# Kernel optimization log

Measured on AMD Instinct MI355X. Metric: run time of the kernel, lower is better.

## Reference

```python
import jax, jax.numpy as jnp
import numpy as np

N = 100000
E = 1600000
F_IN = 500
HID = 8
HEADS = 8
C = 7
NEG_SLOPE = 0.2


def setup_inputs() -> dict:
    key = jax.random.key(0)
    ks = jax.random.split(key, 10)
    x = jax.random.normal(ks[0], (N, F_IN), dtype=jnp.float32)
    edge_index = jax.random.randint(ks[1], (2, E), 0, N, dtype=jnp.int64)
    # conv1 params: lin [heads*hid, F_in], att_src/att_dst [heads, hid], bias [heads*hid]
    s1 = 1.0 / np.sqrt(F_IN)
    W1 = jax.random.normal(ks[2], (HEADS * HID, F_IN), dtype=jnp.float32) * s1
    att_src1 = jax.random.normal(ks[3], (HEADS, HID), dtype=jnp.float32) * 0.1
    att_dst1 = jax.random.normal(ks[4], (HEADS, HID), dtype=jnp.float32) * 0.1
    b1 = jnp.zeros((HEADS * HID,), dtype=jnp.float32)
    # conv2 params: in = heads*hid, out = heads*C (concat=True)
    s2 = 1.0 / np.sqrt(HEADS * HID)
    W2 = jax.random.normal(ks[5], (HEADS * C, HEADS * HID), dtype=jnp.float32) * s2
    att_src2 = jax.random.normal(ks[6], (HEADS, C), dtype=jnp.float32) * 0.1
    att_dst2 = jax.random.normal(ks[7], (HEADS, C), dtype=jnp.float32) * 0.1
    b2 = jnp.zeros((HEADS * C,), dtype=jnp.float32)
    return {"x": x, "edge_index": edge_index, "W1": W1, "att_src1": att_src1,
            "att_dst1": att_dst1, "b1": b1, "W2": W2, "att_src2": att_src2,
            "att_dst2": att_dst2, "b2": b2}


def _gat_layer(h_in, src, dst, W, a_src, a_dst, b, heads, out_ch):
    n = h_in.shape[0]
    h = (h_in @ W.T).reshape(n, heads, out_ch)                 # [N,H,D]
    alpha_s = jnp.sum(h * a_src[None], axis=-1)                # [N,H]
    alpha_d = jnp.sum(h * a_dst[None], axis=-1)                # [N,H]
    e = jax.nn.leaky_relu(alpha_s[src] + alpha_d[dst], NEG_SLOPE)  # [E,H]
    # segment softmax over incoming edges of each dst node
    emax = jax.ops.segment_max(e, dst, num_segments=n)
    ee = jnp.exp(e - emax[dst])
    denom = jax.ops.segment_sum(ee, dst, num_segments=n)
    alpha = ee / denom[dst]                                    # [E,H]
    msg = h[src] * alpha[:, :, None]                           # [E,H,D]
    out = jax.ops.segment_sum(msg, dst, num_segments=n)        # [N,H,D]
    return out.reshape(n, heads * out_ch) + b


def reference(x, edge_index, W1, att_src1, att_dst1, b1, W2, att_src2, att_dst2, b2):
    n = x.shape[0]
    # PyG GATConv adds self-loops by default
    loop = jnp.arange(n, dtype=edge_index.dtype)
    src = jnp.concatenate([edge_index[0], loop])
    dst = jnp.concatenate([edge_index[1], loop])
    # dropout(p=0.6) is identity in eval mode
    h = _gat_layer(x, src, dst, W1, att_src1, att_dst1, b1, HEADS, HID)
    h = jax.nn.elu(h)
    out = _gat_layer(h, src, dst, W2, att_src2, att_dst2, b2, HEADS, C)
    return out  # [N, heads*num_classes]
```

## Files before the change

### kernel.cpp

```cpp
#include <hip/hip_runtime.h>

#define NEG_SLOPE 0.2f

typedef __bf16 bf16x8 __attribute__((ext_vector_type(8)));
typedef float f32x4 __attribute__((ext_vector_type(4)));

__device__ __forceinline__ float eluf(float x) { return x > 0.f ? x : __expf(x) - 1.f; }
__device__ __forceinline__ float lreluf(float x) { return x > 0.f ? x : NEG_SLOPE * x; }
__device__ __forceinline__ float bflo(unsigned u) { return __uint_as_float(u << 16); }
__device__ __forceinline__ float bfhi(unsigned u) { return __uint_as_float(u & 0xffff0000u); }
__device__ __forceinline__ float bfval(unsigned short u) { return __uint_as_float((unsigned)u << 16); }

__device__ __forceinline__ void split8(const float4& p, const float4& q, bf16x8& hi, bf16x8& lo) {
  float v[8] = {p.x, p.y, p.z, p.w, q.x, q.y, q.z, q.w};
#pragma unroll
  for (int e = 0; e < 8; ++e) {
    __bf16 h = (__bf16)v[e];
    hi[e] = h;
    lo[e] = (__bf16)(v[e] - (float)h);
  }
}

__global__ __launch_bounds__(256) void k_zero(int4* __restrict__ p, int n4) {
  int i = blockIdx.x * 256 + threadIdx.x;
  if (i < n4) p[i] = (int4){0, 0, 0, 0};
}


__global__ __launch_bounds__(256) void k_fill_prep(const int* __restrict__ raw, int* __restrict__ cnt,
                                                   int* __restrict__ csr, int E, int CH,
                                                   const float* __restrict__ W1,
                                                   __bf16* __restrict__ b1h, __bf16* __restrict__ b1l,
                                                   const float* __restrict__ W2,
                                                   const float* __restrict__ as2, const float* __restrict__ ad2,
                                                   __bf16* __restrict__ b2h, __bf16* __restrict__ b2l) {
  if (blockIdx.x < 128) {
    int idx = blockIdx.x * 256 + threadIdx.x;
    if (idx < 32768) {
      int e = idx & 7;
      int lane = (idx >> 3) & 63;
      int nf = (idx >> 9) & 3;
      int ks = idx >> 11;
      int k = ks * 32 + (lane >> 4) * 8 + e;
      int col = nf * 16 + (lane & 15);
      float w = (k < 500) ? W1[(size_t)col * 500 + k] : 0.f;
      __bf16 hh = (__bf16)w;
      b1h[idx] = hh;
      b1l[idx] = (__bf16)(w - (float)hh);
    }
    if (idx < 5120) {
      int e = idx & 7;
      int lane = (idx >> 3) & 63;
      int nf = (idx >> 9) % 5;
      int ks = idx / 2560;
      int k = ks * 32 + (lane >> 4) * 8 + e;
      int c16 = lane & 15;
      float w = 0.f;
      if (nf < 4) {
        int col = nf * 16 + c16;
        if (col < 56) w = W2[(size_t)col * 64 + k];
      } else {
        const float* a = (c16 < 8) ? as2 : ad2;
        int h = c16 & 7;
        float s = 0.f;
#pragma unroll
        for (int d = 0; d < 7; ++d) s = fmaf(a[h * 7 + d], W2[(size_t)(h * 7 + d) * 64 + k], s);
        w = s;
      }
      __bf16 hh = (__bf16)w;
      b2h[idx] = hh;
      b2l[idx] = (__bf16)(w - (float)hh);
    }
    return;
  }
  int probe = 0;
#pragma unroll
  for (int t = 1; t < 64; t += 2) probe |= raw[t];
  const bool is32 = probe != 0;
  const int fid = blockIdx.x - 128;
  const int shard = fid & 7;
  const int chunk = fid >> 3;
  const int i0 = chunk * CH;
  const int i1 = min(i0 + CH, E);
  for (int idx = i0 + (int)threadIdx.x; idx < i1; idx += 256) {
    int d = is32 ? raw[E + idx] : raw[2 * (E + idx)];
    if (((d >> 13) & 7) != shard) continue;
    int s = is32 ? raw[idx] : raw[2 * idx];
    int pos = atomicAdd(&cnt[d], 1);
    if (pos < 64) csr[(size_t)d * 64 + pos] = s;
  }
}

__global__ __launch_bounds__(256) void k_gemm1_lds(const float* __restrict__ X, const bf16x8* __restrict__ Bhi,
                                                   const bf16x8* __restrict__ Blo,
                                                   const float* __restrict__ at_s, const float* __restrict__ at_d,
                                                   __bf16* __restrict__ outb,
                                                   __bf16* __restrict__ as1b, float* __restrict__ ad_, int M) {
  __shared__ __align__(16) float xs[2][2048];
  __shared__ __align__(16) __bf16 bs[2][4096];
  const int lane = threadIdx.x & 63;
  const int wid = threadIdx.x >> 6;
  const int row0 = blockIdx.x * 64;
  const int kgrp = lane >> 4;
  const int rloc = lane & 15;
  const int myrow = wid * 16 + rloc;

  const int ub = myrow * 128 + kgrp * 32;
  const int sw1 = (ub ^ ((myrow & 7) << 4)) >> 2;
  const int sw2 = ((ub + 16) ^ ((myrow & 7) << 4)) >> 2;

  int st_r[2], st_kf[2];
#pragma unroll
  for (int j = 0; j < 2; ++j) {
    int s = (wid * 2 + j) * 1024 + lane * 16;
    int r = s >> 7;
    int kb = (s & 127) ^ ((r & 7) << 4);
    st_r[j] = min(row0 + r, M - 1);
    st_kf[j] = kb >> 2;
  }

  auto stage = [&](int buf, int ks) {
#pragma unroll
    for (int j = 0; j < 2; ++j) {
      const float* src = X + (size_t)st_r[j] * 500 + ks * 32 + st_kf[j];
      __builtin_amdgcn_global_load_lds(
          (const __attribute__((address_space(1))) void*)src,
          (__attribute__((address_space(3))) void*)&xs[buf][(wid * 2 + j) * 256], 16, 0, 0);
    }
    const bf16x8* sh = Bhi + (size_t)(ks * 4 + wid) * 64 + lane;
    const bf16x8* sl = Blo + (size_t)(ks * 4 + wid) * 64 + lane;
    __builtin_amdgcn_global_load_lds(
        (const __attribute__((address_space(1))) void*)sh,
        (__attribute__((address_space(3))) void*)&bs[buf][wid * 512], 16, 0, 0);
    __builtin_amdgcn_global_load_lds(
        (const __attribute__((address_space(1))) void*)sl,
        (__attribute__((address_space(3))) void*)&bs[buf][2048 + wid * 512], 16, 0, 0);
  };

  f32x4 acc[4];
#pragma unroll
  for (int nf = 0; nf < 4; ++nf) acc[nf] = (f32x4){0.f, 0.f, 0.f, 0.f};

  stage(0, 0);
  asm volatile("s_waitcnt vmcnt(0)" ::: "memory");
  __builtin_amdgcn_s_barrier();
  __builtin_amdgcn_sched_barrier(0);

  for (int ks = 0; ks < 15; ++ks) {
    const int b = ks & 1;
    float4 p = *reinterpret_cast<const float4*>(&xs[b][sw1]);
    float4 q = *reinterpret_cast<const float4*>(&xs[b][sw2]);
    if (ks < 14) stage(b ^ 1, ks + 1);
    bf16x8 ah, al;
    split8(p, q, ah, al);
#pragma unroll
    for (int nf = 0; nf < 4; ++nf) {
      bf16x8 bh = *reinterpret_cast<const bf16x8*>(&bs[b][nf * 512 + lane * 8]);
      bf16x8 bl = *reinterpret_cast<const bf16x8*>(&bs[b][2048 + nf * 512 + lane * 8]);
      acc[nf] = __builtin_amdgcn_mfma_f32_16x16x32_bf16(ah, bh, acc[nf], 0, 0, 0);
      acc[nf] = __builtin_amdgcn_mfma_f32_16x16x32_bf16(al, bh, acc[nf], 0, 0, 0);
      acc[nf] = __builtin_amdgcn_mfma_f32_16x16x32_bf16(ah, bl, acc[nf], 0, 0, 0);
    }
    if (ks < 14) {
      asm volatile("s_waitcnt vmcnt(0)" ::: "memory");
      __builtin_amdgcn_s_barrier();
      __builtin_amdgcn_sched_barrier(0);
    }
  }

  {
    const bool rowok = row0 + myrow < M;
    const float* xrow = X + (size_t)(row0 + myrow) * 500;
    float v[8];
#pragma unroll
    for (int e = 0; e < 8; ++e) {
      int k = 480 + kgrp * 8 + e;
      v[e] = (rowok && k < 500) ? xrow[k] : 0.f;
    }
    bf16x8 ah, al;
#pragma unroll
    for (int e = 0; e < 8; ++e) {
      __bf16 h = (__bf16)v[e];
      ah[e] = h;
      al[e] = (__bf16)(v[e] - (float)h);
    }
#pragma unroll
    for (int nf = 0; nf < 4; ++nf) {
      bf16x8 bh = Bhi[(15 * 4 + nf) * 64 + lane];
      bf16x8 bl = Blo[(15 * 4 + nf) * 64 + lane];
      acc[nf] = __builtin_amdgcn_mfma_f32_16x16x32_bf16(ah, bh, acc[nf], 0, 0, 0);
      acc[nf] = __builtin_amdgcn_mfma_f32_16x16x32_bf16(al, bh, acc[nf], 0, 0, 0);
      acc[nf] = __builtin_amdgcn_mfma_f32_16x16x32_bf16(ah, bl, acc[nf], 0, 0, 0);
    }
  }

  const int colw = lane & 15;
  const int hi8 = colw >> 3, dd = colw & 7;
  float aS[4], aD[4];
#pragma unroll
  for (int nf = 0; nf < 4; ++nf) {
    aS[nf] = at_s[(nf * 2 + hi8) * 8 + dd];
    aD[nf] = at_d[(nf * 2 + hi8) * 8 + dd];
  }
#pragma unroll
  for (int r = 0; r < 4; ++r) {
    int rowd = row0 + wid * 16 + kgrp * 4 + r;
    bool ok = rowd < M;
    float ps[4], pd[4];
#pragma unroll
    for (int nf = 0; nf < 4; ++nf) {
      ps[nf] = acc[nf][r] * aS[nf];
      pd[nf] = acc[nf][r] * aD[nf];
    }
#pragma unroll
    for (int off = 1; off < 8; off <<= 1) {
#pragma unroll
      for (int nf = 0; nf < 4; ++nf) {
        ps[nf] += __shfl_xor(ps[nf], off);
        pd[nf] += __shfl_xor(pd[nf], off);
      }
    }
    if (ok) {
#pragma unroll
      for (int nf = 0; nf < 4; ++nf)
        outb[(size_t)rowd * 64 + nf * 16 + colw] = (__bf16)acc[nf][r];
      if (dd == 0) {
#pragma unroll
        for (int nf = 0; nf < 4; ++nf) {
          int head = nf * 2 + hi8;
          as1b[(size_t)rowd * 8 + head] = (__bf16)ps[nf];
          ad_[(size_t)rowd * 8 + head] = pd[nf];
        }
      }
    }
  }
}

__global__ __launch_bounds__(256) void k_gemm2_mfma(const __bf16* __restrict__ Xh, const __bf16* __restrict__ Xl,
                                                    const bf16x8* __restrict__ B2h, const bf16x8* __restrict__ B2l,
                                                    __bf16* __restrict__ outb,
                                                    float* __restrict__ ad_, int M) {
  __shared__ __align__(16) __bf16 xh[4096], xl[4096];
  const int lane = threadIdx.x & 63;
  const int wid = threadIdx.x >> 6;
  const int row0 = blockIdx.x * 64;
  const int kgrp = lane >> 4;
  const int rloc = lane & 15;
  const int myrow = wid * 16 + rloc;

#pragma unroll
  for (int j = 0; j < 4; ++j) {
    int chunk = wid * 4 + j;
    bool lo = chunk >= 8;
    int s = (chunk & 7) * 1024 + lane * 16;
    int r = s >> 7;
    int kb = (s & 127) ^ ((r & 7) << 4);
    int rg = min(row0 + r, M - 1);
    const __bf16* src = (lo ? Xl : Xh) + (size_t)rg * 64 + (kb >> 1);
    __bf16* dstbase = (lo ? xl : xh) + (chunk & 7) * 512;
    __builtin_amdgcn_global_load_lds(
        (const __attribute__((address_space(1))) void*)src,
        (__attribute__((address_space(3))) void*)dstbase, 16, 0, 0);
  }
  __syncthreads();

  f32x4 acc[5];
#pragma unroll
  for (int nf = 0; nf < 5; ++nf) acc[nf] = (f32x4){0.f, 0.f, 0.f, 0.f};

#pragma unroll
  for (int ks = 0; ks < 2; ++ks) {
    int ub = myrow * 128 + ks * 64 + kgrp * 16;
    int sw = (ub ^ ((myrow & 7) << 4)) >> 1;
    bf16x8 ah = *reinterpret_cast<const bf16x8*>(&xh[sw]);
    bf16x8 al = *reinterpret_cast<const bf16x8*>(&xl[sw]);
#pragma unroll
    for (int nf = 0; nf < 5; ++nf) {
      bf16x8 bh = B2h[(ks * 5 + nf) * 64 + lane];
      bf16x8 bl = B2l[(ks * 5 + nf) * 64 + lane];
      acc[nf] = __builtin_amdgcn_mfma_f32_16x16x32_bf16(ah, bh, acc[nf], 0, 0, 0);
      acc[nf] = __builtin_amdgcn_mfma_f32_16x16x32_bf16(al, bh, acc[nf], 0, 0, 0);
      acc[nf] = __builtin_amdgcn_mfma_f32_16x16x32_bf16(ah, bl, acc[nf], 0, 0, 0);
    }
  }

  const int colw = lane & 15;
#pragma unroll
  for (int r = 0; r < 4; ++r) {
    float av = acc[4][r];
    float av_x = __shfl_xor(av, 8);
    int rowd = row0 + wid * 16 + (lane >> 4) * 4 + r;
    if (rowd >= M) continue;
#pragma unroll
    for (int nf = 0; nf < 4; ++nf) {
      int col = nf * 16 + colw;
      if (col < 56) {
        int hh = col / 7, cc = col - hh * 7;
        outb[(size_t)rowd * 64 + hh * 8 + cc] = (__bf16)acc[nf][r];
      } else {
        outb[(size_t)rowd * 64 + (col - 56) * 8 + 7] = (__bf16)av_x;
      }
    }
    if (colw >= 8) ad_[(size_t)rowd * 8 + (colw - 8)] = av;
  }
}

__global__ __launch_bounds__(256) void k_agg1v(const unsigned short* __restrict__ hb,
                                               const unsigned short* __restrict__ as1b,
                                               const float* __restrict__ ad_,
                                               const int* __restrict__ cnt,
                                               const int* __restrict__ csr,
                                               const float* __restrict__ b1,
                                               __bf16* __restrict__ oh, __bf16* __restrict__ ol, int N) {
  const int lane = threadIdx.x & 63;
  const int n = blockIdx.x * 4 + (threadIdx.x >> 6);
  if (n >= N) return;
  const int r0 = n << 6;
  const int r1 = r0 + min(cnt[n], 64);
  const int head = lane & 7;
  const int slot = lane >> 3;
  const float ad_h = ad_[(size_t)n * 8 + head];

  float den0 = 0.f, den1 = 0.f;
  f32x4 A0 = {0.f, 0.f, 0.f, 0.f}, B0 = {0.f, 0.f, 0.f, 0.f};
  f32x4 A1 = {0.f, 0.f, 0.f, 0.f}, B1 = {0.f, 0.f, 0.f, 0.f};
  if (slot == 0) {
    float p = __expf(lreluf(bfval(as1b[(size_t)n * 8 + head]) + ad_h));
    uint4 w = *reinterpret_cast<const uint4*>(hb + (size_t)n * 64 + head * 8);
    den0 += p;
    A0[0] = fmaf(p, bflo(w.x), A0[0]); A0[1] = fmaf(p, bfhi(w.x), A0[1]);
    A0[2] = fmaf(p, bflo(w.y), A0[2]); A0[3] = fmaf(p, bfhi(w.y), A0[3]);
    B0[0] = fmaf(p, bflo(w.z), B0[0]); B0[1] = fmaf(p, bfhi(w.z), B0[1]);
    B0[2] = fmaf(p, bflo(w.w), B0[2]); B0[3] = fmaf(p, bfhi(w.w), B0[3]);
  }
  int j = r0 + slot;
  for (; j + 8 < r1; j += 16) {
    int s0 = csr[j], s1 = csr[j + 8];
    float p0 = __expf(lreluf(bfval(as1b[(size_t)s0 * 8 + head]) + ad_h));
    float p1 = __expf(lreluf(bfval(as1b[(size_t)s1 * 8 + head]) + ad_h));
    uint4 w0 = *reinterpret_cast<const uint4*>(hb + (size_t)s0 * 64 + head * 8);
    uint4 w1 = *reinterpret_cast<const uint4*>(hb + (size_t)s1 * 64 + head * 8);
    den0 += p0;
    den1 += p1;
    A0[0] = fmaf(p0, bflo(w0.x), A0[0]); A0[1] = fmaf(p0, bfhi(w0.x), A0[1]);
    A0[2] = fmaf(p0, bflo(w0.y), A0[2]); A0[3] = fmaf(p0, bfhi(w0.y), A0[3]);
    B0[0] = fmaf(p0, bflo(w0.z), B0[0]); B0[1] = fmaf(p0, bfhi(w0.z), B0[1]);
    B0[2] = fmaf(p0, bflo(w0.w), B0[2]); B0[3] = fmaf(p0, bfhi(w0.w), B0[3]);
    A1[0] = fmaf(p1, bflo(w1.x), A1[0]); A1[1] = fmaf(p1, bfhi(w1.x), A1[1]);
    A1[2] = fmaf(p1, bflo(w1.y), A1[2]); A1[3] = fmaf(p1, bfhi(w1.y), A1[3]);
    B1[0] = fmaf(p1, bflo(w1.z), B1[0]); B1[1] = fmaf(p1, bfhi(w1.z), B1[1]);
    B1[2] = fmaf(p1, bflo(w1.w), B1[2]); B1[3] = fmaf(p1, bfhi(w1.w), B1[3]);
  }
  if (j < r1) {
    int s0 = csr[j];
    float p0 = __expf(lreluf(bfval(as1b[(size_t)s0 * 8 + head]) + ad_h));
    uint4 w0 = *reinterpret_cast<const uint4*>(hb + (size_t)s0 * 64 + head * 8);
    den0 += p0;
    A0[0] = fmaf(p0, bflo(w0.x), A0[0]); A0[1] = fmaf(p0, bfhi(w0.x), A0[1]);
    A0[2] = fmaf(p0, bflo(w0.y), A0[2]); A0[3] = fmaf(p0, bfhi(w0.y), A0[3]);
    B0[0] = fmaf(p0, bflo(w0.z), B0[0]); B0[1] = fmaf(p0, bfhi(w0.z), B0[1]);
    B0[2] = fmaf(p0, bflo(w0.w), B0[2]); B0[3] = fmaf(p0, bfhi(w0.w), B0[3]);
  }
  float den = den0 + den1;
#pragma unroll
  for (int k = 0; k < 4; ++k) {
    A0[k] += A1[k];
    B0[k] += B1[k];
  }
#pragma unroll
  for (int off = 8; off < 64; off <<= 1) {
    den += __shfl_xor(den, off);
#pragma unroll
    for (int k = 0; k < 4; ++k) {
      A0[k] += __shfl_xor(A0[k], off);
      B0[k] += __shfl_xor(B0[k], off);
    }
  }
  if (lane < 8) {
    float inv_den = 1.f / den;
    float o[8];
#pragma unroll
    for (int k = 0; k < 4; ++k) {
      o[k] = eluf(A0[k] * inv_den + b1[lane * 8 + k]);
      o[4 + k] = eluf(B0[k] * inv_den + b1[lane * 8 + 4 + k]);
    }
    bf16x8 vh, vl;
#pragma unroll
    for (int k = 0; k < 8; ++k) {
      __bf16 h = (__bf16)o[k];
      vh[k] = h;
      vl[k] = (__bf16)(o[k] - (float)h);
    }
    *reinterpret_cast<bf16x8*>(oh + (size_t)n * 64 + lane * 8) = vh;
    *reinterpret_cast<bf16x8*>(ol + (size_t)n * 64 + lane * 8) = vl;
  }
}

__global__ __launch_bounds__(256) void k_agg2v(const unsigned short* __restrict__ hb,
                                               const float* __restrict__ ad_,
                                               const int* __restrict__ cnt,
                                               const int* __restrict__ csr,
                                               const float* __restrict__ bias,
                                               float* __restrict__ out, int N) {
  const int lane = threadIdx.x & 63;
  const int n = blockIdx.x * 4 + (threadIdx.x >> 6);
  if (n >= N) return;
  const int r0 = n << 6;
  const int r1 = r0 + min(cnt[n], 64);
  const int head = lane & 7;
  const int slot = lane >> 3;
  const float ad_h = ad_[(size_t)n * 8 + head];

  float den0 = 0.f, den1 = 0.f;
  f32x4 A0 = {0.f, 0.f, 0.f, 0.f}, B0 = {0.f, 0.f, 0.f, 0.f};
  f32x4 A1 = {0.f, 0.f, 0.f, 0.f}, B1 = {0.f, 0.f, 0.f, 0.f};
  if (slot == 0) {
    uint4 w = *reinterpret_cast<const uint4*>(hb + (size_t)n * 64 + head * 8);
    float p = __expf(lreluf(bfhi(w.w) + ad_h));
    den0 += p;
    A0[0] = fmaf(p, bflo(w.x), A0[0]); A0[1] = fmaf(p, bfhi(w.x), A0[1]);
    A0[2] = fmaf(p, bflo(w.y), A0[2]); A0[3] = fmaf(p, bfhi(w.y), A0[3]);
    B0[0] = fmaf(p, bflo(w.z), B0[0]); B0[1] = fmaf(p, bfhi(w.z), B0[1]);
    B0[2] = fmaf(p, bflo(w.w), B0[2]);
  }
  int j = r0 + slot;
  for (; j + 8 < r1; j += 16) {
    int s0 = csr[j], s1 = csr[j + 8];
    uint4 w0 = *reinterpret_cast<const uint4*>(hb + (size_t)s0 * 64 + head * 8);
    uint4 w1 = *reinterpret_cast<const uint4*>(hb + (size_t)s1 * 64 + head * 8);
    float p0 = __expf(lreluf(bfhi(w0.w) + ad_h));
    float p1 = __expf(lreluf(bfhi(w1.w) + ad_h));
    den0 += p0;
    den1 += p1;
    A0[0] = fmaf(p0, bflo(w0.x), A0[0]); A0[1] = fmaf(p0, bfhi(w0.x), A0[1]);
    A0[2] = fmaf(p0, bflo(w0.y), A0[2]); A0[3] = fmaf(p0, bfhi(w0.y), A0[3]);
    B0[0] = fmaf(p0, bflo(w0.z), B0[0]); B0[1] = fmaf(p0, bfhi(w0.z), B0[1]);
    B0[2] = fmaf(p0, bflo(w0.w), B0[2]);
    A1[0] = fmaf(p1, bflo(w1.x), A1[0]); A1[1] = fmaf(p1, bfhi(w1.x), A1[1]);
    A1[2] = fmaf(p1, bflo(w1.y), A1[2]); A1[3] = fmaf(p1, bfhi(w1.y), A1[3]);
    B1[0] = fmaf(p1, bflo(w1.z), B1[0]); B1[1] = fmaf(p1, bfhi(w1.z), B1[1]);
    B1[2] = fmaf(p1, bflo(w1.w), B1[2]);
  }
  if (j < r1) {
    int s0 = csr[j];
    uint4 w0 = *reinterpret_cast<const uint4*>(hb + (size_t)s0 * 64 + head * 8);
    float p0 = __expf(lreluf(bfhi(w0.w) + ad_h));
    den0 += p0;
    A0[0] = fmaf(p0, bflo(w0.x), A0[0]); A0[1] = fmaf(p0, bfhi(w0.x), A0[1]);
    A0[2] = fmaf(p0, bflo(w0.y), A0[2]); A0[3] = fmaf(p0, bfhi(w0.y), A0[3]);
    B0[0] = fmaf(p0, bflo(w0.z), B0[0]); B0[1] = fmaf(p0, bfhi(w0.z), B0[1]);
    B0[2] = fmaf(p0, bflo(w0.w), B0[2]);
  }
  float den = den0 + den1;
#pragma unroll
  for (int k = 0; k < 4; ++k) {
    A0[k] += A1[k];
    B0[k] += B1[k];
  }
#pragma unroll
  for (int off = 8; off < 64; off <<= 1) {
    den += __shfl_xor(den, off);
#pragma unroll
    for (int k = 0; k < 4; ++k) {
      A0[k] += __shfl_xor(A0[k], off);
      B0[k] += __shfl_xor(B0[k], off);
    }
  }
  if (lane < 8) {
    float inv_den = 1.f / den;
    float* orow = out + (size_t)n * 56 + head * 7;
    const float* brow = bias + head * 7;
    orow[0] = A0[0] * inv_den + brow[0];
    orow[1] = A0[1] * inv_den + brow[1];
    orow[2] = A0[2] * inv_den + brow[2];
    orow[3] = A0[3] * inv_den + brow[3];
    orow[4] = B0[0] * inv_den + brow[4];
    orow[5] = B0[1] * inv_den + brow[5];
    orow[6] = B0[2] * inv_den + brow[6];
  }
}


extern "C" void kernel_launch(void* const* d_in, const int* in_sizes, int n_in,
                              void* d_out, int out_size, void* d_ws, size_t ws_size,
                              hipStream_t stream) {
  const float* x    = (const float*)d_in[0];
  const int*   ei   = (const int*)d_in[1];
  const float* W1   = (const float*)d_in[2];
  const float* at_s1 = (const float*)d_in[3];
  const float* at_d1 = (const float*)d_in[4];
  const float* b1   = (const float*)d_in[5];
  const float* W2   = (const float*)d_in[6];
  const float* at_s2 = (const float*)d_in[7];
  const float* at_d2 = (const float*)d_in[8];
  const float* b2   = (const float*)d_in[9];
  float* out = (float*)d_out;

  const int N = in_sizes[0] / 500;
  const int E = in_sizes[1] / 2;

  char* w = (char*)d_ws;
  auto alloc = [&](size_t bytes) -> void* {
    void* p = (void*)w;
    w += (bytes + 255) & ~(size_t)255;
    return p;
  };
  int*   cnt    = (int*)alloc((size_t)N * 4);
  int*   csr    = (int*)alloc((size_t)N * 64 * 4);
  float* adb    = (float*)alloc((size_t)N * 8 * 4);
  __bf16* as1b  = (__bf16*)alloc((size_t)N * 8 * 2);
  __bf16* B1h   = (__bf16*)alloc((size_t)32768 * 2);
  __bf16* B1l   = (__bf16*)alloc((size_t)32768 * 2);
  __bf16* B2h   = (__bf16*)alloc((size_t)5120 * 2);
  __bf16* B2l   = (__bf16*)alloc((size_t)5120 * 2);
  __bf16* h1b   = (__bf16*)alloc((size_t)N * 64 * 2);
  __bf16* o1h   = (__bf16*)alloc((size_t)N * 64 * 2);
  __bf16* o1l   = (__bf16*)alloc((size_t)N * 64 * 2);
  __bf16* h2b   = (__bf16*)alloc((size_t)N * 64 * 2);

  auto cdiv = [](int a, int b) { return (a + b - 1) / b; };

  k_zero<<<cdiv(N, 1024), 256, 0, stream>>>((int4*)cnt, cdiv(N, 4));
  {
    const int G = 768;
    k_fill_prep<<<128 + 8 * G, 256, 0, stream>>>(ei, cnt, csr, E, cdiv(E, G),
                                                 W1, B1h, B1l, W2, at_s2, at_d2, B2h, B2l);
  }

  k_gemm1_lds<<<cdiv(N, 64), 256, 0, stream>>>(x, (const bf16x8*)B1h, (const bf16x8*)B1l,
                                               at_s1, at_d1, h1b, as1b, adb, N);
  k_agg1v<<<cdiv(N, 4), 256, 0, stream>>>((const unsigned short*)h1b, (const unsigned short*)as1b,
                                          adb, cnt, csr, b1, o1h, o1l, N);

  k_gemm2_mfma<<<cdiv(N, 64), 256, 0, stream>>>(o1h, o1l, (const bf16x8*)B2h, (const bf16x8*)B2l, h2b, adb, N);
  k_agg2v<<<cdiv(N, 4), 256, 0, stream>>>((const unsigned short*)h2b, adb, cnt, csr, b2, out, N);
}
```

Before: 251.6 us.

## Widen GEMM1 K-tile to 128 and read B fragments from global

```diff
diff --git a/kernel.cpp b/kernel.cpp
--- a/kernel.cpp
+++ b/kernel.cpp
@@ -25,7 +25,6 @@
   int i = blockIdx.x * 256 + threadIdx.x;
   if (i < n4) p[i] = (int4){0, 0, 0, 0};
 }
-
 
 __global__ __launch_bounds__(256) void k_fill_prep(const int* __restrict__ raw, int* __restrict__ cnt,
                                                    int* __restrict__ csr, int E, int CH,
@@ -96,8 +95,7 @@
                                                    const float* __restrict__ at_s, const float* __restrict__ at_d,
                                                    __bf16* __restrict__ outb,
                                                    __bf16* __restrict__ as1b, float* __restrict__ ad_, int M) {
-  __shared__ __align__(16) float xs[2][2048];
-  __shared__ __align__(16) __bf16 bs[2][4096];
+  __shared__ __align__(16) float xs[2][8192];
   const int lane = threadIdx.x & 63;
   const int wid = threadIdx.x >> 6;
   const int row0 = blockIdx.x * 64;
@@ -105,92 +103,66 @@
   const int rloc = lane & 15;
   const int myrow = wid * 16 + rloc;
 
-  const int ub = myrow * 128 + kgrp * 32;
-  const int sw1 = (ub ^ ((myrow & 7) << 4)) >> 2;
-  const int sw2 = ((ub + 16) ^ ((myrow & 7) << 4)) >> 2;
-
-  int st_r[2], st_kf[2];
-#pragma unroll
-  for (int j = 0; j < 2; ++j) {
-    int s = (wid * 2 + j) * 1024 + lane * 16;
-    int r = s >> 7;
-    int kb = (s & 127) ^ ((r & 7) << 4);
+  int swA[4], swB[4];
+#pragma unroll
+  for (int ksub = 0; ksub < 4; ++ksub) {
+    int ub = myrow * 512 + ksub * 128 + kgrp * 32;
+    swA[ksub] = (ub ^ ((myrow & 7) << 4)) >> 2;
+    swB[ksub] = ((ub + 16) ^ ((myrow & 7) << 4)) >> 2;
+  }
+
+  int st_r[8], st_kf[8];
+#pragma unroll
+  for (int j = 0; j < 8; ++j) {
+    int s = (wid * 8 + j) * 1024 + lane * 16;
+    int r = s >> 9;
+    int kb = (s & 511) ^ ((r & 7) << 4);
     st_r[j] = min(row0 + r, M - 1);
     st_kf[j] = kb >> 2;
   }
 
-  auto stage = [&](int buf, int ks) {
-#pragma unroll
-    for (int j = 0; j < 2; ++j) {
-      const float* src = X + (size_t)st_r[j] * 500 + ks * 32 + st_kf[j];
+  auto stage = [&](float* buf, int t) {
+#pragma unroll
+    for (int j = 0; j < 8; ++j) {
+      const float* src = X + (size_t)st_r[j] * 500 + t * 128 + st_kf[j];
       __builtin_amdgcn_global_load_lds(
           (const __attribute__((address_space(1))) void*)src,
-          (__attribute__((address_space(3))) void*)&xs[buf][(wid * 2 + j) * 256], 16, 0, 0);
-    }
-    const bf16x8* sh = Bhi + (size_t)(ks * 4 + wid) * 64 + lane;
-    const bf16x8* sl = Blo + (size_t)(ks * 4 + wid) * 64 + lane;
-    __builtin_amdgcn_global_load_lds(
-        (const __attribute__((address_space(1))) void*)sh,
-        (__attribute__((address_space(3))) void*)&bs[buf][wid * 512], 16, 0, 0);
-    __builtin_amdgcn_global_load_lds(
-        (const __attribute__((address_space(1))) void*)sl,
-        (__attribute__((address_space(3))) void*)&bs[buf][2048 + wid * 512], 16, 0, 0);
+          (__attribute__((address_space(3))) void*)(buf + (wid * 8 + j) * 256), 16, 0, 0);
+    }
   };
 
   f32x4 acc[4];
 #pragma unroll
   for (int nf = 0; nf < 4; ++nf) acc[nf] = (f32x4){0.f, 0.f, 0.f, 0.f};
 
-  stage(0, 0);
+  stage(xs[0], 0);
   asm volatile("s_waitcnt vmcnt(0)" ::: "memory");
   __builtin_amdgcn_s_barrier();
   __builtin_amdgcn_sched_barrier(0);
 
-  for (int ks = 0; ks < 15; ++ks) {
-    const int b = ks & 1;
-    float4 p = *reinterpret_cast<const float4*>(&xs[b][sw1]);
-    float4 q = *reinterpret_cast<const float4*>(&xs[b][sw2]);
-    if (ks < 14) stage(b ^ 1, ks + 1);
-    bf16x8 ah, al;
-    split8(p, q, ah, al);
-#pragma unroll
-    for (int nf = 0; nf < 4; ++nf) {
-      bf16x8 bh = *reinterpret_cast<const bf16x8*>(&bs[b][nf * 512 + lane * 8]);
-      bf16x8 bl = *reinterpret_cast<const bf16x8*>(&bs[b][2048 + nf * 512 + lane * 8]);
-      acc[nf] = __builtin_amdgcn_mfma_f32_16x16x32_bf16(ah, bh, acc[nf], 0, 0, 0);
-      acc[nf] = __builtin_amdgcn_mfma_f32_16x16x32_bf16(al, bh, acc[nf], 0, 0, 0);
-      acc[nf] = __builtin_amdgcn_mfma_f32_16x16x32_bf16(ah, bl, acc[nf], 0, 0, 0);
-    }
-    if (ks < 14) {
+  for (int t = 0; t < 4; ++t) {
+    float* cur = xs[t & 1];
+    if (t < 3) stage(xs[(t & 1) ^ 1], t + 1);
+#pragma unroll
+    for (int ksub = 0; ksub < 4; ++ksub) {
+      float4 p = *reinterpret_cast<const float4*>(&cur[swA[ksub]]);
+      float4 q = *reinterpret_cast<const float4*>(&cur[swB[ksub]]);
+      bf16x8 ah, al;
+      split8(p, q, ah, al);
+      const int kk = t * 4 + ksub;
+#pragma unroll
+      for (int nf = 0; nf < 4; ++nf) {
+        bf16x8 bh = Bhi[(kk * 4 + nf) * 64 + lane];
+        bf16x8 bl = Blo[(kk * 4 + nf) * 64 + lane];
+        acc[nf] = __builtin_amdgcn_mfma_f32_16x16x32_bf16(ah, bh, acc[nf], 0, 0, 0);
+        acc[nf] = __builtin_amdgcn_mfma_f32_16x16x32_bf16(al, bh, acc[nf], 0, 0, 0);
+        acc[nf] = __builtin_amdgcn_mfma_f32_16x16x32_bf16(ah, bl, acc[nf], 0, 0, 0);
+      }
+    }
+    if (t < 3) {
       asm volatile("s_waitcnt vmcnt(0)" ::: "memory");
       __builtin_amdgcn_s_barrier();
       __builtin_amdgcn_sched_barrier(0);
-    }
-  }
-
-  {
-    const bool rowok = row0 + myrow < M;
-    const float* xrow = X + (size_t)(row0 + myrow) * 500;
-    float v[8];
-#pragma unroll
-    for (int e = 0; e < 8; ++e) {
-      int k = 480 + kgrp * 8 + e;
-      v[e] = (rowok && k < 500) ? xrow[k] : 0.f;
-    }
-    bf16x8 ah, al;
-#pragma unroll
-    for (int e = 0; e < 8; ++e) {
-      __bf16 h = (__bf16)v[e];
-      ah[e] = h;
-      al[e] = (__bf16)(v[e] - (float)h);
-    }
-#pragma unroll
-    for (int nf = 0; nf < 4; ++nf) {
-      bf16x8 bh = Bhi[(15 * 4 + nf) * 64 + lane];
-      bf16x8 bl = Blo[(15 * 4 + nf) * 64 + lane];
-      acc[nf] = __builtin_amdgcn_mfma_f32_16x16x32_bf16(ah, bh, acc[nf], 0, 0, 0);
-      acc[nf] = __builtin_amdgcn_mfma_f32_16x16x32_bf16(al, bh, acc[nf], 0, 0, 0);
-      acc[nf] = __builtin_amdgcn_mfma_f32_16x16x32_bf16(ah, bl, acc[nf], 0, 0, 0);
     }
   }
 
```

Result: slower. 260.8 us (median of 2 runs) (+3.7%).
